# Kernel tuning notes

Hardware: AMD Instinct MI355X
Metric: run time of the kernel (lower is better)

The kernel has to match this reference:

```python
import jax, jax.numpy as jnp
import numpy as np

B, T, D, H = 16, 512, 512, 16
DH = D // H
P = 2 * T - 1  # relative position length


def _conv2d_same(x, w, b):
    # x: [B,C,H,W], w: [O,I,3,3]
    y = jax.lax.conv_general_dilated(x, w, (1, 1), 'SAME',
                                     dimension_numbers=('NCHW', 'OIHW', 'NCHW'))
    return y + b[None, :, None, None]


def _relative_shift(ps):
    # ps: [B,H,T,P] -> pad, reshape trick, keep first P//2+1 == T columns
    b, h, t, p = ps.shape
    ps = jnp.pad(ps, ((0, 0), (0, 0), (0, 0), (1, 0)))
    ps = ps.reshape(b, h, p + 1, t)[:, :, 1:].reshape(b, h, t, p)
    return ps[..., : p // 2 + 1]


def setup_inputs() -> dict:
    key = jax.random.key(0)
    ks = jax.random.split(key, 20)
    s = 0.02
    return {
        'query': jax.random.normal(ks[0], (B, T, D), jnp.float32),
        'key': jax.random.normal(ks[1], (B, T, D), jnp.float32),
        'value': jax.random.normal(ks[2], (B, T, D), jnp.float32),
        'pos_embedding': jax.random.normal(ks[3], (B, P, D), jnp.float32),
        'mask': jax.random.bernoulli(ks[4], 0.1, (B, 1, T)),
        'bpp': jax.random.uniform(ks[5], (B, T, T), jnp.float32),
        'Wq': jax.random.normal(ks[6], (D, D), jnp.float32) * s,
        'bq': jnp.zeros((D,), jnp.float32),
        'Wk': jax.random.normal(ks[7], (D, D), jnp.float32) * s,
        'bk': jnp.zeros((D,), jnp.float32),
        'Wv': jax.random.normal(ks[8], (D, D), jnp.float32) * s,
        'bv': jnp.zeros((D,), jnp.float32),
        'Wp': jax.random.normal(ks[9], (D, D), jnp.float32) * s,
        'Wo': jax.random.normal(ks[10], (D, D), jnp.float32) * s,
        'bo': jnp.zeros((D,), jnp.float32),
        'u_bias': jax.random.normal(ks[11], (H, DH), jnp.float32) * s,
        'v_bias': jax.random.normal(ks[12], (H, DH), jnp.float32) * s,
        'c1w': jax.random.normal(ks[13], (16, 1, 3, 3), jnp.float32) * s,
        'c1b': jnp.zeros((16,), jnp.float32),
        'c2w': jax.random.normal(ks[14], (1, 16, 3, 3), jnp.float32) * s,
        'c2b': jnp.zeros((1,), jnp.float32),
    }


def reference(query, key, value, pos_embedding, mask, bpp,
              Wq, bq, Wk, bk, Wv, bv, Wp, Wo, bo,
              u_bias, v_bias, c1w, c1b, c2w, c2b):
    b = value.shape[0]
    # bpp-derived bias: [B,1,T,T]
    h1 = jax.nn.relu(_conv2d_same(bpp[:, None], c1w, c1b))
    bpp_bias = _conv2d_same(h1, c2w, c2b)  # broadcasts over heads

    q = (query @ Wq.T + bq).reshape(b, -1, H, DH)          # [B,T,H,dh]
    k = (key @ Wk.T + bk).reshape(b, -1, H, DH)            # [B,T,H,dh]
    v = (value @ Wv.T + bv).reshape(b, -1, H, DH)          # [B,T,H,dh]
    p = (pos_embedding @ Wp) .reshape(b, -1, H, DH) if False else (pos_embedding @ Wp.T).reshape(b, -1, H, DH)  # [B,P,H,dh]

    content_score = jnp.einsum('bthd,bshd->bhts', q + u_bias, k)
    pos_score = jnp.einsum('bthd,bphd->bhtp', q + v_bias, p)
    pos_score = _relative_shift(pos_score)                 # [B,H,T,T]

    score = (content_score + pos_score) / jnp.sqrt(jnp.asarray(DH, score_dtype := content_score.dtype)) + bpp_bias
    score = jnp.where(mask[:, None], jnp.asarray(-10000.0, score.dtype), score)
    attn = jax.nn.softmax(score, axis=-1)                  # dropout_p=0 (eval)

    ctx = jnp.einsum('bhts,bshd->bthd', attn, v).reshape(b, -1, D)
    return ctx @ Wo.T + bo
```

## Files before the change

### kernel.cpp

```cpp
#include <hip/hip_runtime.h>

constexpr int Bn  = 16;
constexpr int Tn  = 512;
constexpr int Dn  = 512;
constexpr int Hn  = 16;
constexpr int DHn = 32;
constexpr int Pn  = 1023;
constexpr size_t wE = (size_t)Dn * Dn;

typedef __attribute__((ext_vector_type(8))) short s16x8;
typedef __attribute__((ext_vector_type(4))) float f32x4;

__device__ __forceinline__ unsigned short f2bf(float x) {
    unsigned u = __float_as_uint(x);
    unsigned r = u + 0x7fff + ((u >> 16) & 1);
    return (unsigned short)(r >> 16);
}
__device__ __forceinline__ float bf2f(unsigned short h) {
    return __uint_as_float(((unsigned)h) << 16);
}

__device__ __forceinline__ f32x4 mfma3(s16x8 ah, s16x8 al, s16x8 bh2, s16x8 bl, f32x4 c) {
    c = __builtin_amdgcn_mfma_f32_16x16x32_bf16(ah, bh2, c, 0, 0, 0);
    c = __builtin_amdgcn_mfma_f32_16x16x32_bf16(ah, bl,  c, 0, 0, 0);
    c = __builtin_amdgcn_mfma_f32_16x16x32_bf16(al, bh2, c, 0, 0, 0);
    return c;
}

__global__ __launch_bounds__(256) void split_weights_kernel(
    const float* __restrict__ w0, const float* __restrict__ w1,
    const float* __restrict__ w2, const float* __restrict__ w3,
    const float* __restrict__ w4,
    unsigned short* __restrict__ hi, unsigned short* __restrict__ lo) {
    const float* srcs[5] = {w0, w1, w2, w3, w4};
    const float* src = srcs[blockIdx.y];
    const size_t off = (size_t)blockIdx.y * wE;
    unsigned short* h = hi + off;
    unsigned short* l = lo + off;
    const int n4 = Dn * Dn / 4;
    for (int i = blockIdx.x * 256 + threadIdx.x; i < n4; i += 64 * 256) {
        float4 v = ((const float4*)src)[i];
        ushort4 hh, ll;
        hh.x = f2bf(v.x); ll.x = f2bf(v.x - bf2f(hh.x));
        hh.y = f2bf(v.y); ll.y = f2bf(v.y - bf2f(hh.y));
        hh.z = f2bf(v.z); ll.z = f2bf(v.z - bf2f(hh.z));
        hh.w = f2bf(v.w); ll.w = f2bf(v.w - bf2f(hh.w));
        ((ushort4*)h)[i] = hh;
        ((ushort4*)l)[i] = ll;
    }
}

__global__ void mask_decode_kernel(const unsigned char* __restrict__ mraw,
                                   float* __restrict__ mout) {
    __shared__ int s_nonmod4;
    __shared__ int s_big;
    if (threadIdx.x == 0) { s_nonmod4 = 0; s_big = 0; }
    __syncthreads();
    int f0 = 0, f1 = 0;
    for (int i = threadIdx.x; i < Bn * Tn; i += 256) {
        unsigned char v = mraw[i];
        if ((i & 3) != 0 && v != 0) f0 = 1;
        if (v > 1) f1 = 1;
    }
    if (f0) atomicOr(&s_nonmod4, 1);
    if (f1) atomicOr(&s_big, 1);
    __syncthreads();
    const int layout = s_big ? 2 : (s_nonmod4 ? 1 : 0);
    for (int i = threadIdx.x; i < Bn * Tn; i += 256) {
        bool m;
        if (layout == 2)      m = ((const float*)mraw)[i] != 0.0f;
        else if (layout == 1) m = mraw[i] != 0;
        else                  m = ((const int*)mraw)[i] != 0;
        mout[i] = m ? 1.0f : 0.0f;
    }
}

__global__ __launch_bounds__(256) void conv_bias_kernel(
    const float* __restrict__ bpp, const float* __restrict__ c1w,
    const float* __restrict__ c1b, const float* __restrict__ c2w,
    const float* __restrict__ c2b, unsigned short* __restrict__ biasout) {
    const int x0 = blockIdx.x * 64, y0 = blockIdx.y * 64, b = blockIdx.z;
    __shared__ __align__(16) float inb[68][72];
    __shared__ __align__(16) float h1[66][72];
    __shared__ float w1s[16][9], w2s[16][9], b1s[16];
    const int tid = threadIdx.x;
    const int tx = tid & 15, ty = tid >> 4;

    if (tid < 144) { w1s[tid / 9][tid % 9] = c1w[tid]; w2s[tid / 9][tid % 9] = c2w[tid]; }
    if (tid < 16) b1s[tid] = c1b[tid];
    const float* src = bpp + (size_t)b * Tn * Tn;
    for (int i = tid; i < 68 * 18; i += 256) {
        const int r = i / 18, cq = i % 18;
        const int gy = y0 - 2 + r, gx = x0 - 4 + cq * 4;
        float4 v = make_float4(0.f, 0.f, 0.f, 0.f);
        if (gy >= 0 && gy < Tn && gx >= 0 && gx < Tn)
            v = *(const float4*)(src + (size_t)gy * Tn + gx);
        *(float4*)&inb[r][cq * 4] = v;
    }
    __syncthreads();

    float acc[4][4] = {};
    for (int ch = 0; ch < 16; ++ch) {
        if (ch) __syncthreads();
        float w1r[9], w2r[9];
#pragma unroll
        for (int k = 0; k < 9; ++k) { w1r[k] = w1s[ch][k]; w2r[k] = w2s[ch][k]; }
        const float b1v = b1s[ch];
        for (int i = tid; i < 66 * 17; i += 256) {
            const int rr = i / 17, q = i % 17;
            float v[3][8];
#pragma unroll
            for (int dy = 0; dy < 3; ++dy) {
                float4 p0 = *(const float4*)&inb[rr + dy][q * 4];
                float4 p1 = *(const float4*)&inb[rr + dy][q * 4 + 4];
                v[dy][0] = p0.x; v[dy][1] = p0.y; v[dy][2] = p0.z; v[dy][3] = p0.w;
                v[dy][4] = p1.x; v[dy][5] = p1.y; v[dy][6] = p1.z; v[dy][7] = p1.w;
            }
            const int gy = y0 + rr - 1;
            const int gxb = x0 + q * 4 - 1;
            const bool rowok = (gy >= 0 && gy < Tn);
            float o4[4];
#pragma unroll
            for (int j = 0; j < 4; ++j) {
                float s = b1v;
#pragma unroll
                for (int dy = 0; dy < 3; ++dy)
#pragma unroll
                    for (int dx = 0; dx < 3; ++dx)
                        s += v[dy][2 + j + dx] * w1r[dy * 3 + dx];
                const int gx = gxb + j;
                o4[j] = (rowok && gx >= 0 && gx < Tn) ? fmaxf(s, 0.0f) : 0.0f;
            }
            *(float4*)&h1[rr][q * 4] = make_float4(o4[0], o4[1], o4[2], o4[3]);
        }
        __syncthreads();
        float h[6][6];
#pragma unroll
        for (int r6 = 0; r6 < 6; ++r6) {
            float4 a = *(const float4*)&h1[ty * 4 + r6][tx * 4];
            float2 b2 = *(const float2*)&h1[ty * 4 + r6][tx * 4 + 4];
            h[r6][0] = a.x; h[r6][1] = a.y; h[r6][2] = a.z; h[r6][3] = a.w;
            h[r6][4] = b2.x; h[r6][5] = b2.y;
        }
#pragma unroll
        for (int i2 = 0; i2 < 4; ++i2)
#pragma unroll
            for (int j = 0; j < 4; ++j) {
                float s = 0.0f;
#pragma unroll
                for (int dy = 0; dy < 3; ++dy)
#pragma unroll
                    for (int dx = 0; dx < 3; ++dx)
                        s += h[i2 + dy][j + dx] * w2r[dy * 3 + dx];
                acc[i2][j] += s;
            }
    }
    const float ob = c2b[0];
#pragma unroll
    for (int i2 = 0; i2 < 4; ++i2) {
        ushort4 o;
        o.x = f2bf(acc[i2][0] + ob); o.y = f2bf(acc[i2][1] + ob);
        o.z = f2bf(acc[i2][2] + ob); o.w = f2bf(acc[i2][3] + ob);
        *(ushort4*)(biasout + ((size_t)b * Tn + y0 + ty * 4 + i2) * Tn + x0 + tx * 4) = o;
    }
}

template<int NT>
__device__ __forceinline__ void gemm_body(
    const float* __restrict__ A,
    const unsigned short* __restrict__ Wh, const unsigned short* __restrict__ Wl,
    const float* __restrict__ bias, float* __restrict__ outf,
    unsigned short* __restrict__ out_hi, unsigned short* __restrict__ out_lo,
    int M, int L, int mode, int nbase, int mbase) {
    constexpr int K = 512, BK = 32, LDT = 40, NW = NT / 32;
    constexpr int WC = (NT * BK) / (256 * 8);
    __shared__ __align__(16) unsigned short AhT[128 * LDT];
    __shared__ __align__(16) unsigned short AlT[128 * LDT];
    __shared__ __align__(16) unsigned short WhT[NT * LDT];
    __shared__ __align__(16) unsigned short WlT[NT * LDT];
    const int tid = threadIdx.x;
    const int wave = tid >> 6, lane = tid & 63;
    const int wr = wave >> 1, wc = wave & 1;
    const int lg = lane >> 4, lr = lane & 15;
    f32x4 acc[4][NW] = {};

    float4 pa0[2], pa1[2];
    s16x8 pwh[WC], pwl[WC];
    auto issue_loads = [&](int k0) {
#pragma unroll
        for (int c = 0; c < 2; ++c) {
            const int cid = tid + 256 * c;
            const int row = cid >> 2, col8 = (cid & 3) * 8;
            int gm = mbase + row; if (gm >= M) gm = M - 1;
            const float* ap = A + (size_t)gm * K + k0 + col8;
            pa0[c] = *(const float4*)ap;
            pa1[c] = *(const float4*)(ap + 4);
        }
#pragma unroll
        for (int c = 0; c < WC; ++c) {
            const int cid = tid + 256 * c;
            const int row = cid >> 2, col8 = (cid & 3) * 8;
            const size_t gw = (size_t)(nbase + row) * K + k0 + col8;
            pwh[c] = *(const s16x8*)&Wh[gw];
            pwl[c] = *(const s16x8*)&Wl[gw];
        }
    };
    issue_loads(0);
    for (int ks = 0; ks < K / BK; ++ks) {
        const int k0 = ks * BK;
        __syncthreads();
#pragma unroll
        for (int c = 0; c < 2; ++c) {
            const int cid = tid + 256 * c;
            const int row = cid >> 2, col8 = (cid & 3) * 8;
            float av[8] = {pa0[c].x, pa0[c].y, pa0[c].z, pa0[c].w,
                           pa1[c].x, pa1[c].y, pa1[c].z, pa1[c].w};
            s16x8 hh, ll;
#pragma unroll
            for (int j = 0; j < 8; ++j) {
                unsigned short x = f2bf(av[j]);
                hh[j] = (short)x;
                ll[j] = (short)f2bf(av[j] - bf2f(x));
            }
            const int loff = row * LDT + col8;
            *(s16x8*)&AhT[loff] = hh;
            *(s16x8*)&AlT[loff] = ll;
        }
#pragma unroll
        for (int c = 0; c < WC; ++c) {
            const int cid = tid + 256 * c;
            const int loff = (cid >> 2) * LDT + (cid & 3) * 8;
            *(s16x8*)&WhT[loff] = pwh[c];
            *(s16x8*)&WlT[loff] = pwl[c];
        }
        if (ks < K / BK - 1) issue_loads(k0 + BK);
        __syncthreads();
        s16x8 wh[NW], wl[NW];
#pragma unroll
        for (int nj = 0; nj < NW; ++nj) {
            const int off = (wc * (NT / 2) + nj * 16 + lr) * LDT + lg * 8;
            wh[nj] = *(const s16x8*)&WhT[off];
            wl[nj] = *(const s16x8*)&WlT[off];
        }
#pragma unroll
        for (int mi = 0; mi < 4; ++mi) {
            const int off = (wr * 64 + mi * 16 + lr) * LDT + lg * 8;
            s16x8 ah = *(const s16x8*)&AhT[off];
            s16x8 al = *(const s16x8*)&AlT[off];
#pragma unroll
            for (int nj = 0; nj < NW; ++nj)
                acc[mi][nj] = __builtin_amdgcn_mfma_f32_16x16x32_bf16(ah, wh[nj], acc[mi][nj], 0, 0, 0);
#pragma unroll
            for (int nj = 0; nj < NW; ++nj)
                acc[mi][nj] = __builtin_amdgcn_mfma_f32_16x16x32_bf16(ah, wl[nj], acc[mi][nj], 0, 0, 0);
#pragma unroll
            for (int nj = 0; nj < NW; ++nj)
                acc[mi][nj] = __builtin_amdgcn_mfma_f32_16x16x32_bf16(al, wh[nj], acc[mi][nj], 0, 0, 0);
        }
    }
#pragma unroll
    for (int nj = 0; nj < NW; ++nj) {
        const int n = nbase + wc * (NT / 2) + nj * 16 + lr;
        const float bv = bias ? bias[n] : 0.0f;
#pragma unroll
        for (int mi = 0; mi < 4; ++mi) {
#pragma unroll
            for (int r2 = 0; r2 < 4; ++r2) {
                const int m = mbase + wr * 64 + mi * 16 + lg * 4 + r2;
                if (m < M) {
                    const float v = acc[mi][nj][r2] + bv;
                    if (mode == 0) {
                        outf[(size_t)m * 512 + n] = v;
                    } else if (mode == 1) {
                        int bb = m / L, t = m - bb * L;
                        int hh2 = n >> 5, d = n & 31;
                        outf[(((size_t)bb * Hn + hh2) * L + t) * DHn + d] = v;
                    } else {
                        int bb = m / L, t = m - bb * L;
                        int hh2 = n >> 5, d = n & 31;
                        size_t oidx = (mode == 2)
                            ? ((((size_t)bb * Hn + hh2) * L + t) * DHn + d)
                            : ((((size_t)bb * Hn + hh2) * DHn + d) * L + t);
                        unsigned short hi16 = f2bf(v);
                        out_hi[oidx] = hi16;
                        out_lo[oidx] = f2bf(v - bf2f(hi16));
                    }
                }
            }
        }
    }
}

__global__ __launch_bounds__(256, 3) void gemm_qkvp_kernel(
    const float* __restrict__ q, const float* __restrict__ k,
    const float* __restrict__ v, const float* __restrict__ p,
    const unsigned short* __restrict__ wall_hi, const unsigned short* __restrict__ wall_lo,
    const float* __restrict__ bq, const float* __restrict__ bk,
    const float* __restrict__ bv,
    float* __restrict__ q_ws,
    unsigned short* __restrict__ k_hi, unsigned short* __restrict__ k_lo,
    unsigned short* __restrict__ v_hi, unsigned short* __restrict__ v_lo,
    unsigned short* __restrict__ p_hi, unsigned short* __restrict__ p_lo) {
    const int bid = blockIdx.x;
    const int swz = (bid & 7) * 160 + (bid >> 3);
    int z, mblk, nblk;
    if (swz < 768) { z = swz >> 8; const int r = swz & 255; mblk = r >> 2; nblk = r & 3; }
    else           { z = 3; const int r = swz - 768;        mblk = r >> 2; nblk = r & 3; }
    const float* A; const float* bias = nullptr;
    float* outf = nullptr; unsigned short *ohi = nullptr, *olo = nullptr;
    int M, L, mode;
    if (z == 0)      { A = q; bias = bq; outf = q_ws; M = Bn * Tn; L = Tn; mode = 1; }
    else if (z == 1) { A = k; bias = bk; ohi = k_hi; olo = k_lo; M = Bn * Tn; L = Tn; mode = 2; }
    else if (z == 2) { A = v; bias = bv; ohi = v_hi; olo = v_lo; M = Bn * Tn; L = Tn; mode = 3; }
    else             { A = p; ohi = p_hi; olo = p_lo; M = Bn * Pn; L = Pn; mode = 2; }
    gemm_body<128>(A, wall_hi + (size_t)z * wE, wall_lo + (size_t)z * wE, bias,
                   outf, ohi, olo, M, L, mode, nblk * 128, mblk * 128);
}

__global__ __launch_bounds__(256, 3) void gemm_o_kernel(
    const float* __restrict__ A,
    const unsigned short* __restrict__ Wh, const unsigned short* __restrict__ Wl,
    const float* __restrict__ bias, float* __restrict__ out) {
    const int bid = blockIdx.x;
    const int swz = (bid & 7) * 64 + (bid >> 3);
    const int nbase = (swz & 7) * 64;
    const int mbase = (swz >> 3) * 128;
    gemm_body<64>(A, Wh, Wl, bias, out, nullptr, nullptr,
                  Bn * Tn, Tn, 0, nbase, mbase);
}

__global__ __launch_bounds__(256, 2) void attn_mfma_kernel(
    const float* __restrict__ q_ws,
    const unsigned short* __restrict__ k_hi, const unsigned short* __restrict__ k_lo,
    const unsigned short* __restrict__ vt_hi, const unsigned short* __restrict__ vt_lo,
    const unsigned short* __restrict__ p_hi, const unsigned short* __restrict__ p_lo,
    const unsigned short* __restrict__ biasw, const float* __restrict__ maskw,
    const float* __restrict__ ub, const float* __restrict__ vb,
    float* __restrict__ ctx) {
    const int bid = blockIdx.x;
    const int wg = ((bid & 7) << 9) | (bid >> 3);
    const int t0 = (wg & 15) * 32;
    const int h = (wg >> 4) & 15;
    const int b = wg >> 8;
    const int tid = threadIdx.x;
    const int w = tid >> 6, l = tid & 63;
    const int lr = l & 15, lg = l >> 4;
    const size_t bh = (size_t)b * Hn + h;
    const int pbase = 480 - t0;
    const float scale = 0.17677669529663687f;

    __shared__ __align__(16) char uni[4][8192];
    __shared__ float redbuf[2][32][4];
    char* ubase = uni[w];

    s16x8 quh[2], qul[2], qvh[2], qvl[2];
#pragma unroll
    for (int i = 0; i < 2; ++i) {
        const float* qrow = q_ws + (bh * Tn + t0 + 16 * i + lr) * DHn + lg * 8;
        float4 qa = *(const float4*)qrow;
        float4 qb = *(const float4*)(qrow + 4);
        float qv8[8] = {qa.x, qa.y, qa.z, qa.w, qb.x, qb.y, qb.z, qb.w};
#pragma unroll
        for (int j = 0; j < 8; ++j) {
            const float uj = ub[h * DHn + lg * 8 + j];
            const float vj = vb[h * DHn + lg * 8 + j];
            float xu = qv8[j] + uj;
            unsigned short hu = f2bf(xu);
            quh[i][j] = (short)hu; qul[i][j] = (short)f2bf(xu - bf2f(hu));
            float xv = qv8[j] + vj;
            unsigned short hv = f2bf(xv);
            qvh[i][j] = (short)hv; qvl[i][j] = (short)f2bf(xv - bf2f(hv));
        }
    }
    float mv[8];
#pragma unroll
    for (int m = 0; m < 8; ++m)
        mv[m] = maskw[b * Tn + w * 128 + m * 16 + lr];

    auto posTile = [&](int i, int jt) -> f32x4 {
        int pidx = pbase + w * 128 + jt * 16 + lr;
        if (pidx > Pn - 1) pidx = Pn - 1;
        const size_t po = (bh * Pn + pidx) * DHn + lg * 8;
        s16x8 ph = *(const s16x8*)(p_hi + po);
        s16x8 pl = *(const s16x8*)(p_lo + po);
        f32x4 t = {0.f, 0.f, 0.f, 0.f};
        return mfma3(qvh[i], qvl[i], ph, pl, t);
    };

    f32x4 sc[2][8];
    f32x4 p0a = posTile(0, 1);
    f32x4 p1a = posTile(1, 0);
    const int ubb = lr - 4 * lg + 31;

#pragma unroll
    for (int m = 0; m < 8; ++m) {
        f32x4 p0b = posTile(0, m + 2);
        f32x4 p1b = posTile(1, m + 1);
        float bvls[2][4];
#pragma unroll
        for (int i2 = 0; i2 < 2; ++i2)
#pragma unroll
            for (int r2 = 0; r2 < 4; ++r2)
                bvls[i2][r2] = bf2f(biasw[((size_t)b * Tn + t0 + 16 * i2 + 4 * lg + r2) * Tn
                                          + w * 128 + m * 16 + lr]);
        const size_t ko = (bh * Tn + w * 128 + m * 16 + lr) * DHn + lg * 8;
        s16x8 kh = *(const s16x8*)(k_hi + ko);
        s16x8 kl = *(const s16x8*)(k_lo + ko);
#pragma unroll
        for (int i = 0; i < 2; ++i) {
            f32x4 c = {0.f, 0.f, 0.f, 0.f};
            c = mfma3(quh[i], qul[i], kh, kl, c);
            f32x4 Pa = (i == 0) ? p0a : p1a;
            f32x4 Pb = (i == 0) ? p0b : p1b;
            f32x4 out;
#pragma unroll
            for (int r2 = 0; r2 < 4; ++r2) {
                const int u = ubb - r2;
                const int src = (l & 48) | (u & 15);
                float pa = __shfl(Pa[r2], src, 64);
                float pb = __shfl(Pb[r2], src, 64);
                float pv = (u < 32) ? pa : pb;
                float v = (c[r2] + pv) * scale + bvls[i][r2];
                if (mv[m] != 0.0f) v = -10000.0f;
                out[r2] = v;
            }
            sc[i][m] = out;
        }
        p0a = p0b; p1a = p1b;
    }

    float rowm[2][4], inv[2][4];
#pragma unroll
    for (int i = 0; i < 2; ++i)
#pragma unroll
        for (int r2 = 0; r2 < 4; ++r2) {
            float mx = -1e30f;
#pragma unroll
            for (int m = 0; m < 8; ++m) mx = fmaxf(mx, sc[i][m][r2]);
#pragma unroll
            for (int off = 1; off < 16; off <<= 1) mx = fmaxf(mx, __shfl_xor(mx, off, 64));
            if (lr == 0) redbuf[0][16 * i + 4 * lg + r2][w] = mx;
        }
    __syncthreads();
#pragma unroll
    for (int i = 0; i < 2; ++i)
#pragma unroll
        for (int r2 = 0; r2 < 4; ++r2) {
            float4 mm = *(const float4*)redbuf[0][16 * i + 4 * lg + r2];
            rowm[i][r2] = fmaxf(fmaxf(mm.x, mm.y), fmaxf(mm.z, mm.w));
        }
    float psum[2][4] = {};
#pragma unroll
    for (int i = 0; i < 2; ++i)
#pragma unroll
        for (int m = 0; m < 8; ++m)
#pragma unroll
            for (int r2 = 0; r2 < 4; ++r2) {
                float e = __expf(sc[i][m][r2] - rowm[i][r2]);
                sc[i][m][r2] = e;
                psum[i][r2] += e;
            }
#pragma unroll
    for (int i = 0; i < 2; ++i)
#pragma unroll
        for (int r2 = 0; r2 < 4; ++r2) {
            float s = psum[i][r2];
#pragma unroll
            for (int off = 1; off < 16; off <<= 1) s += __shfl_xor(s, off, 64);
            if (lr == 0) redbuf[1][16 * i + 4 * lg + r2][w] = s;
        }
    __syncthreads();
#pragma unroll
    for (int i = 0; i < 2; ++i)
#pragma unroll
        for (int r2 = 0; r2 < 4; ++r2) {
            float4 ss = *(const float4*)redbuf[1][16 * i + 4 * lg + r2];
            inv[i][r2] = 1.0f / (ss.x + ss.y + ss.z + ss.w);
        }

    f32x4 cacc[2][2] = {};
#pragma unroll
    for (int sh = 0; sh < 2; ++sh) {
#pragma unroll
        for (int mm2 = 0; mm2 < 4; ++mm2) {
            const int m = sh * 4 + mm2;
#pragma unroll
            for (int i = 0; i < 2; ++i)
#pragma unroll
                for (int r2 = 0; r2 < 4; ++r2) {
                    const int trow = 16 * i + 4 * lg + r2;
                    float a = sc[i][m][r2] * inv[i][r2];
                    unsigned short ah16 = f2bf(a);
                    unsigned short al16 = f2bf(a - bf2f(ah16));
                    const int cbyte = (mm2 * 16 + lr) * 2;
                    const int off = trow * 128 + (cbyte ^ ((trow & 7) << 4));
                    *(unsigned short*)(ubase + off) = ah16;
                    *(unsigned short*)(ubase + 4096 + off) = al16;
                }
        }
#pragma unroll
        for (int ks = 0; ks < 2; ++ks) {
            s16x8 pah[2], pal[2];
#pragma unroll
            for (int i = 0; i < 2; ++i) {
                const int trow = 16 * i + lr;
                const int cbyte = ks * 64 + lg * 16;
                const int off = trow * 128 + (cbyte ^ ((trow & 7) << 4));
                pah[i] = *(const s16x8*)(ubase + off);
                pal[i] = *(const s16x8*)(ubase + 4096 + off);
            }
#pragma unroll
            for (int n = 0; n < 2; ++n) {
                const int sg = w * 128 + sh * 64 + ks * 32 + lg * 8;
                const size_t vo = (bh * DHn + n * 16 + lr) * Tn + sg;
                s16x8 vh = *(const s16x8*)(vt_hi + vo);
                s16x8 vl = *(const s16x8*)(vt_lo + vo);
#pragma unroll
                for (int i = 0; i < 2; ++i)
                    cacc[i][n] = mfma3(pah[i], pal[i], vh, vl, cacc[i][n]);
            }
        }
    }

    {
        float* cr = (float*)ubase;
#pragma unroll
        for (int i = 0; i < 2; ++i)
#pragma unroll
            for (int n = 0; n < 2; ++n)
#pragma unroll
                for (int r2 = 0; r2 < 4; ++r2)
                    cr[(16 * i + 4 * lg + r2) * 36 + n * 16 + lr] = cacc[i][n][r2];
    }
    __syncthreads();
    {
        const int trow = tid >> 3, d0 = (tid & 7) * 4;
        float4 s0 = *(const float4*)((float*)uni[0] + trow * 36 + d0);
        float4 s1 = *(const float4*)((float*)uni[1] + trow * 36 + d0);
        float4 s2 = *(const float4*)((float*)uni[2] + trow * 36 + d0);
        float4 s3 = *(const float4*)((float*)uni[3] + trow * 36 + d0);
        float4 o = make_float4(s0.x + s1.x + s2.x + s3.x, s0.y + s1.y + s2.y + s3.y,
                               s0.z + s1.z + s2.z + s3.z, s0.w + s1.w + s2.w + s3.w);
        *(float4*)(ctx + ((size_t)b * Tn + t0 + trow) * Dn + h * DHn + d0) = o;
    }
}

extern "C" void kernel_launch(void* const* d_in, const int* in_sizes, int n_in,
                              void* d_out, int out_size, void* d_ws, size_t ws_size,
                              hipStream_t stream) {
    const float* query = (const float*)d_in[0];
    const float* key   = (const float*)d_in[1];
    const float* value = (const float*)d_in[2];
    const float* pos   = (const float*)d_in[3];
    const unsigned char* mask = (const unsigned char*)d_in[4];
    const float* bpp = (const float*)d_in[5];
    const float* Wq = (const float*)d_in[6];
    const float* bq = (const float*)d_in[7];
    const float* Wk = (const float*)d_in[8];
    const float* bk = (const float*)d_in[9];
    const float* Wv = (const float*)d_in[10];
    const float* bv = (const float*)d_in[11];
    const float* Wp = (const float*)d_in[12];
    const float* Wo = (const float*)d_in[13];
    const float* bo = (const float*)d_in[14];
    const float* ub = (const float*)d_in[15];
    const float* vbias = (const float*)d_in[16];
    const float* c1w = (const float*)d_in[17];
    const float* c1b = (const float*)d_in[18];
    const float* c2w = (const float*)d_in[19];
    const float* c2b = (const float*)d_in[20];

    const size_t qkvE = (size_t)Bn * Hn * Tn * DHn;
    const size_t posE = (size_t)Bn * Hn * Pn * DHn;

    char* wsb = (char*)d_ws;
    unsigned short* bias_ws = (unsigned short*)wsb;
    float* mask_ws = (float*)(wsb + sizeof(unsigned short) * (size_t)Bn * Tn * Tn);
    float* q_ws    = mask_ws + Bn * Tn;
    float* ctx_ws  = q_ws + qkvE;
    unsigned short* k_hi = (unsigned short*)(ctx_ws + (size_t)Bn * Tn * Dn);
    unsigned short* k_lo = k_hi + qkvE;
    unsigned short* v_hi = k_lo + qkvE;
    unsigned short* v_lo = v_hi + qkvE;
    unsigned short* p_hi = v_lo + qkvE;
    unsigned short* p_lo = p_hi + posE;
    unsigned short* wall_hi = p_lo + posE;
    unsigned short* wall_lo = wall_hi + 5 * wE;

    split_weights_kernel<<<dim3(64, 5), dim3(256), 0, stream>>>(
        Wq, Wk, Wv, Wp, Wo, wall_hi, wall_lo);
    mask_decode_kernel<<<dim3(1), dim3(256), 0, stream>>>(mask, mask_ws);
    conv_bias_kernel<<<dim3(8, 8, Bn), dim3(256), 0, stream>>>(
        bpp, c1w, c1b, c2w, c2b, bias_ws);

    gemm_qkvp_kernel<<<dim3(1280), dim3(256), 0, stream>>>(
        query, key, value, pos, wall_hi, wall_lo, bq, bk, bv,
        q_ws, k_hi, k_lo, v_hi, v_lo, p_hi, p_lo);

    attn_mfma_kernel<<<dim3(4096), dim3(256), 0, stream>>>(
        q_ws, k_hi, k_lo, v_hi, v_lo, p_hi, p_lo, bias_ws, mask_ws, ub, vbias, ctx_ws);

    gemm_o_kernel<<<dim3(512), dim3(256), 0, stream>>>(
        ctx_ws, wall_hi + 4 * wE, wall_lo + 4 * wE, bo, (float*)d_out);
}
```

Measured before the change: 416.3 us.

## Merge conv bias, mask decode and QKVP GEMM into one launch

Folds the bpp convolution kernel and the mask decode kernel into the QKVP projection kernel as extra blocks, using a shared-memory arena overlaid between the GEMM and conv layouts. This removes two launches and lets the conv work fill idle CUs during the GEMM tail. In exchange, the conv blocks now run under the GEMM's launch bounds and shared memory size, which may change their occupancy and register allocation. The single mask block can also land at the end of the grid.

```diff
diff --git a/kernel.cpp b/kernel.cpp
--- a/kernel.cpp
+++ b/kernel.cpp
@@ -50,123 +50,23 @@
     }
 }
 
-__global__ void mask_decode_kernel(const unsigned char* __restrict__ mraw,
-                                   float* __restrict__ mout) {
-    __shared__ int s_nonmod4;
-    __shared__ int s_big;
-    if (threadIdx.x == 0) { s_nonmod4 = 0; s_big = 0; }
-    __syncthreads();
-    int f0 = 0, f1 = 0;
-    for (int i = threadIdx.x; i < Bn * Tn; i += 256) {
-        unsigned char v = mraw[i];
-        if ((i & 3) != 0 && v != 0) f0 = 1;
-        if (v > 1) f1 = 1;
-    }
-    if (f0) atomicOr(&s_nonmod4, 1);
-    if (f1) atomicOr(&s_big, 1);
-    __syncthreads();
-    const int layout = s_big ? 2 : (s_nonmod4 ? 1 : 0);
-    for (int i = threadIdx.x; i < Bn * Tn; i += 256) {
-        bool m;
-        if (layout == 2)      m = ((const float*)mraw)[i] != 0.0f;
-        else if (layout == 1) m = mraw[i] != 0;
-        else                  m = ((const int*)mraw)[i] != 0;
-        mout[i] = m ? 1.0f : 0.0f;
-    }
-}
-
-__global__ __launch_bounds__(256) void conv_bias_kernel(
-    const float* __restrict__ bpp, const float* __restrict__ c1w,
-    const float* __restrict__ c1b, const float* __restrict__ c2w,
-    const float* __restrict__ c2b, unsigned short* __restrict__ biasout) {
-    const int x0 = blockIdx.x * 64, y0 = blockIdx.y * 64, b = blockIdx.z;
-    __shared__ __align__(16) float inb[68][72];
-    __shared__ __align__(16) float h1[66][72];
-    __shared__ float w1s[16][9], w2s[16][9], b1s[16];
-    const int tid = threadIdx.x;
-    const int tx = tid & 15, ty = tid >> 4;
-
-    if (tid < 144) { w1s[tid / 9][tid % 9] = c1w[tid]; w2s[tid / 9][tid % 9] = c2w[tid]; }
-    if (tid < 16) b1s[tid] = c1b[tid];
-    const float* src = bpp + (size_t)b * Tn * Tn;
-    for (int i = tid; i < 68 * 18; i += 256) {
-        const int r = i / 18, cq = i % 18;
-        const int gy = y0 - 2 + r, gx = x0 - 4 + cq * 4;
-        float4 v = make_float4(0.f, 0.f, 0.f, 0.f);
-        if (gy >= 0 && gy < Tn && gx >= 0 && gx < Tn)
-            v = *(const float4*)(src + (size_t)gy * Tn + gx);
-        *(float4*)&inb[r][cq * 4] = v;
-    }
-    __syncthreads();
-
-    float acc[4][4] = {};
-    for (int ch = 0; ch < 16; ++ch) {
-        if (ch) __syncthreads();
-        float w1r[9], w2r[9];
-#pragma unroll
-        for (int k = 0; k < 9; ++k) { w1r[k] = w1s[ch][k]; w2r[k] = w2s[ch][k]; }
-        const float b1v = b1s[ch];
-        for (int i = tid; i < 66 * 17; i += 256) {
-            const int rr = i / 17, q = i % 17;
-            float v[3][8];
-#pragma unroll
-            for (int dy = 0; dy < 3; ++dy) {
-                float4 p0 = *(const float4*)&inb[rr + dy][q * 4];
-                float4 p1 = *(const float4*)&inb[rr + dy][q * 4 + 4];
-                v[dy][0] = p0.x; v[dy][1] = p0.y; v[dy][2] = p0.z; v[dy][3] = p0.w;
-                v[dy][4] = p1.x; v[dy][5] = p1.y; v[dy][6] = p1.z; v[dy][7] = p1.w;
-            }
-            const int gy = y0 + rr - 1;
-            const int gxb = x0 + q * 4 - 1;
-            const bool rowok = (gy >= 0 && gy < Tn);
-            float o4[4];
-#pragma unroll
-            for (int j = 0; j < 4; ++j) {
-                float s = b1v;
-#pragma unroll
-                for (int dy = 0; dy < 3; ++dy)
-#pragma unroll
-                    for (int dx = 0; dx < 3; ++dx)
-                        s += v[dy][2 + j + dx] * w1r[dy * 3 + dx];
-                const int gx = gxb + j;
-                o4[j] = (rowok && gx >= 0 && gx < Tn) ? fmaxf(s, 0.0f) : 0.0f;
-            }
-            *(float4*)&h1[rr][q * 4] = make_float4(o4[0], o4[1], o4[2], o4[3]);
-        }
-        __syncthreads();
-        float h[6][6];
-#pragma unroll
-        for (int r6 = 0; r6 < 6; ++r6) {
-            float4 a = *(const float4*)&h1[ty * 4 + r6][tx * 4];
-            float2 b2 = *(const float2*)&h1[ty * 4 + r6][tx * 4 + 4];
-            h[r6][0] = a.x; h[r6][1] = a.y; h[r6][2] = a.z; h[r6][3] = a.w;
-            h[r6][4] = b2.x; h[r6][5] = b2.y;
-        }
-#pragma unroll
-        for (int i2 = 0; i2 < 4; ++i2)
-#pragma unroll
-            for (int j = 0; j < 4; ++j) {
-                float s = 0.0f;
-#pragma unroll
-                for (int dy = 0; dy < 3; ++dy)
-#pragma unroll
-                    for (int dx = 0; dx < 3; ++dx)
-                        s += h[i2 + dy][j + dx] * w2r[dy * 3 + dx];
-                acc[i2][j] += s;
-            }
-    }
-    const float ob = c2b[0];
-#pragma unroll
-    for (int i2 = 0; i2 < 4; ++i2) {
-        ushort4 o;
-        o.x = f2bf(acc[i2][0] + ob); o.y = f2bf(acc[i2][1] + ob);
-        o.z = f2bf(acc[i2][2] + ob); o.w = f2bf(acc[i2][3] + ob);
-        *(ushort4*)(biasout + ((size_t)b * Tn + y0 + ty * 4 + i2) * Tn + x0 + tx * 4) = o;
-    }
-}
+struct GemmSmem {
+    unsigned short AhT[128 * 40];
+    unsigned short AlT[128 * 40];
+    unsigned short WhT[128 * 40];
+    unsigned short WlT[128 * 40];
+};
+struct ConvSmem {
+    float inb[68][72];
+    float h1[66][72];
+    float w1s[16][9], w2s[16][9], b1s[16];
+};
+static_assert(sizeof(ConvSmem) <= sizeof(GemmSmem), "arena too small");
 
 template<int NT>
 __device__ __forceinline__ void gemm_body(
+    unsigned short* __restrict__ AhT, unsigned short* __restrict__ AlT,
+    unsigned short* __restrict__ WhT, unsigned short* __restrict__ WlT,
     const float* __restrict__ A,
     const unsigned short* __restrict__ Wh, const unsigned short* __restrict__ Wl,
     const float* __restrict__ bias, float* __restrict__ outf,
@@ -174,10 +74,6 @@
     int M, int L, int mode, int nbase, int mbase) {
     constexpr int K = 512, BK = 32, LDT = 40, NW = NT / 32;
     constexpr int WC = (NT * BK) / (256 * 8);
-    __shared__ __align__(16) unsigned short AhT[128 * LDT];
-    __shared__ __align__(16) unsigned short AlT[128 * LDT];
-    __shared__ __align__(16) unsigned short WhT[NT * LDT];
-    __shared__ __align__(16) unsigned short WlT[NT * LDT];
     const int tid = threadIdx.x;
     const int wave = tid >> 6, lane = tid & 63;
     const int wr = wave >> 1, wc = wave & 1;
@@ -291,7 +187,7 @@
     }
 }
 
-__global__ __launch_bounds__(256, 3) void gemm_qkvp_kernel(
+__global__ __launch_bounds__(256, 3) void phase1_kernel(
     const float* __restrict__ q, const float* __restrict__ k,
     const float* __restrict__ v, const float* __restrict__ p,
     const unsigned short* __restrict__ wall_hi, const unsigned short* __restrict__ wall_lo,
@@ -300,32 +196,157 @@
     float* __restrict__ q_ws,
     unsigned short* __restrict__ k_hi, unsigned short* __restrict__ k_lo,
     unsigned short* __restrict__ v_hi, unsigned short* __restrict__ v_lo,
-    unsigned short* __restrict__ p_hi, unsigned short* __restrict__ p_lo) {
+    unsigned short* __restrict__ p_hi, unsigned short* __restrict__ p_lo,
+    const float* __restrict__ bpp, const float* __restrict__ c1w,
+    const float* __restrict__ c1b, const float* __restrict__ c2w,
+    const float* __restrict__ c2b, unsigned short* __restrict__ biasout,
+    const unsigned char* __restrict__ mraw, float* __restrict__ mout) {
+    __shared__ __align__(16) char arena[sizeof(GemmSmem)];
     const int bid = blockIdx.x;
-    const int swz = (bid & 7) * 160 + (bid >> 3);
-    int z, mblk, nblk;
-    if (swz < 768) { z = swz >> 8; const int r = swz & 255; mblk = r >> 2; nblk = r & 3; }
-    else           { z = 3; const int r = swz - 768;        mblk = r >> 2; nblk = r & 3; }
-    const float* A; const float* bias = nullptr;
-    float* outf = nullptr; unsigned short *ohi = nullptr, *olo = nullptr;
-    int M, L, mode;
-    if (z == 0)      { A = q; bias = bq; outf = q_ws; M = Bn * Tn; L = Tn; mode = 1; }
-    else if (z == 1) { A = k; bias = bk; ohi = k_hi; olo = k_lo; M = Bn * Tn; L = Tn; mode = 2; }
-    else if (z == 2) { A = v; bias = bv; ohi = v_hi; olo = v_lo; M = Bn * Tn; L = Tn; mode = 3; }
-    else             { A = p; ohi = p_hi; olo = p_lo; M = Bn * Pn; L = Pn; mode = 2; }
-    gemm_body<128>(A, wall_hi + (size_t)z * wE, wall_lo + (size_t)z * wE, bias,
-                   outf, ohi, olo, M, L, mode, nblk * 128, mblk * 128);
+    const int tid = threadIdx.x;
+
+    if (bid < 1280) {
+        GemmSmem* gs = (GemmSmem*)arena;
+        const int swz = (bid & 7) * 160 + (bid >> 3);
+        int z, mblk, nblk;
+        if (swz < 768) { z = swz >> 8; const int r = swz & 255; mblk = r >> 2; nblk = r & 3; }
+        else           { z = 3; const int r = swz - 768;        mblk = r >> 2; nblk = r & 3; }
+        const float* A; const float* bias = nullptr;
+        float* outf = nullptr; unsigned short *ohi = nullptr, *olo = nullptr;
+        int M, L, mode;
+        if (z == 0)      { A = q; bias = bq; outf = q_ws; M = Bn * Tn; L = Tn; mode = 1; }
+        else if (z == 1) { A = k; bias = bk; ohi = k_hi; olo = k_lo; M = Bn * Tn; L = Tn; mode = 2; }
+        else if (z == 2) { A = v; bias = bv; ohi = v_hi; olo = v_lo; M = Bn * Tn; L = Tn; mode = 3; }
+        else             { A = p; ohi = p_hi; olo = p_lo; M = Bn * Pn; L = Pn; mode = 2; }
+        gemm_body<128>(gs->AhT, gs->AlT, gs->WhT, gs->WlT,
+                       A, wall_hi + (size_t)z * wE, wall_lo + (size_t)z * wE, bias,
+                       outf, ohi, olo, M, L, mode, nblk * 128, mblk * 128);
+        return;
+    }
+    if (bid < 1280 + 1024) {
+        ConvSmem* cs = (ConvSmem*)arena;
+        const int cid = bid - 1280;
+        const int b = cid >> 6, rem = cid & 63;
+        const int x0 = (rem & 7) * 64, y0 = (rem >> 3) * 64;
+        const int tx = tid & 15, ty = tid >> 4;
+
+        if (tid < 144) { cs->w1s[tid / 9][tid % 9] = c1w[tid]; cs->w2s[tid / 9][tid % 9] = c2w[tid]; }
+        if (tid < 16) cs->b1s[tid] = c1b[tid];
+        const float* src = bpp + (size_t)b * Tn * Tn;
+        for (int i = tid; i < 68 * 18; i += 256) {
+            const int r = i / 18, cq = i % 18;
+            const int gy = y0 - 2 + r, gx = x0 - 4 + cq * 4;
+            float4 vv = make_float4(0.f, 0.f, 0.f, 0.f);
+            if (gy >= 0 && gy < Tn && gx >= 0 && gx < Tn)
+                vv = *(const float4*)(src + (size_t)gy * Tn + gx);
+            *(float4*)&cs->inb[r][cq * 4] = vv;
+        }
+        __syncthreads();
+
+        float acc[4][4] = {};
+        for (int ch = 0; ch < 16; ++ch) {
+            if (ch) __syncthreads();
+            float w1r[9], w2r[9];
+#pragma unroll
+            for (int kk = 0; kk < 9; ++kk) { w1r[kk] = cs->w1s[ch][kk]; w2r[kk] = cs->w2s[ch][kk]; }
+            const float b1v = cs->b1s[ch];
+            for (int i = tid; i < 66 * 17; i += 256) {
+                const int rr = i / 17, qq = i % 17;
+                float vv[3][8];
+#pragma unroll
+                for (int dy = 0; dy < 3; ++dy) {
+                    float4 p0 = *(const float4*)&cs->inb[rr + dy][qq * 4];
+                    float4 p1 = *(const float4*)&cs->inb[rr + dy][qq * 4 + 4];
+                    vv[dy][0] = p0.x; vv[dy][1] = p0.y; vv[dy][2] = p0.z; vv[dy][3] = p0.w;
+                    vv[dy][4] = p1.x; vv[dy][5] = p1.y; vv[dy][6] = p1.z; vv[dy][7] = p1.w;
+                }
+                const int gy = y0 + rr - 1;
+                const int gxb = x0 + qq * 4 - 1;
+                const bool rowok = (gy >= 0 && gy < Tn);
+                float o4[4];
+#pragma unroll
+                for (int j = 0; j < 4; ++j) {
+                    float s = b1v;
+#pragma unroll
+                    for (int dy = 0; dy < 3; ++dy)
+#pragma unroll
+                        for (int dx = 0; dx < 3; ++dx)
+                            s += vv[dy][2 + j + dx] * w1r[dy * 3 + dx];
+                    const int gx = gxb + j;
+                    o4[j] = (rowok && gx >= 0 && gx < Tn) ? fmaxf(s, 0.0f) : 0.0f;
+                }
+                *(float4*)&cs->h1[rr][qq * 4] = make_float4(o4[0], o4[1], o4[2], o4[3]);
+            }
+            __syncthreads();
+            float hh[6][6];
+#pragma unroll
+            for (int r6 = 0; r6 < 6; ++r6) {
+                float4 a = *(const float4*)&cs->h1[ty * 4 + r6][tx * 4];
+                float2 b2 = *(const float2*)&cs->h1[ty * 4 + r6][tx * 4 + 4];
+                hh[r6][0] = a.x; hh[r6][1] = a.y; hh[r6][2] = a.z; hh[r6][3] = a.w;
+                hh[r6][4] = b2.x; hh[r6][5] = b2.y;
+            }
+#pragma unroll
+            for (int i2 = 0; i2 < 4; ++i2)
+#pragma unroll
+                for (int j = 0; j < 4; ++j) {
+                    float s = 0.0f;
+#pragma unroll
+                    for (int dy = 0; dy < 3; ++dy)
+#pragma unroll
+                        for (int dx = 0; dx < 3; ++dx)
+                            s += hh[i2 + dy][j + dx] * w2r[dy * 3 + dx];
+                    acc[i2][j] += s;
+                }
+        }
+        const float ob = c2b[0];
+#pragma unroll
+        for (int i2 = 0; i2 < 4; ++i2) {
+            ushort4 o;
+            o.x = f2bf(acc[i2][0] + ob); o.y = f2bf(acc[i2][1] + ob);
+            o.z = f2bf(acc[i2][2] + ob); o.w = f2bf(acc[i2][3] + ob);
+            *(ushort4*)(biasout + ((size_t)b * Tn + y0 + ty * 4 + i2) * Tn + x0 + tx * 4) = o;
+        }
+        return;
+    }
+    {
+        int* flags = (int*)arena;
+        if (tid == 0) { flags[0] = 0; flags[1] = 0; }
+        __syncthreads();
+        int f0 = 0, f1 = 0;
+        for (int i = tid; i < Bn * Tn; i += 256) {
+            unsigned char vv = mraw[i];
+            if ((i & 3) != 0 && vv != 0) f0 = 1;
+            if (vv > 1) f1 = 1;
+        }
+        if (f0) atomicOr(&flags[0], 1);
+        if (f1) atomicOr(&flags[1], 1);
+        __syncthreads();
+        const int layout = flags[1] ? 2 : (flags[0] ? 1 : 0);
+        for (int i = tid; i < Bn * Tn; i += 256) {
+            bool m;
+            if (layout == 2)      m = ((const float*)mraw)[i] != 0.0f;
+            else if (layout == 1) m = mraw[i] != 0;
+            else                  m = ((const int*)mraw)[i] != 0;
+            mout[i] = m ? 1.0f : 0.0f;
+        }
+    }
 }
 
 __global__ __launch_bounds__(256, 3) void gemm_o_kernel(
     const float* __restrict__ A,
     const unsigned short* __restrict__ Wh, const unsigned short* __restrict__ Wl,
     const float* __restrict__ bias, float* __restrict__ out) {
+    constexpr int LDT = 40;
+    __shared__ __align__(16) unsigned short AhT[128 * LDT];
+    __shared__ __align__(16) unsigned short AlT[128 * LDT];
+    __shared__ __align__(16) unsigned short WhT[64 * LDT];
+    __shared__ __align__(16) unsigned short WlT[64 * LDT];
     const int bid = blockIdx.x;
     const int swz = (bid & 7) * 64 + (bid >> 3);
     const int nbase = (swz & 7) * 64;
     const int mbase = (swz >> 3) * 128;
-    gemm_body<64>(A, Wh, Wl, bias, out, nullptr, nullptr,
+    gemm_body<64>(AhT, AlT, WhT, WlT, A, Wh, Wl, bias, out, nullptr, nullptr,
                   Bn * Tn, Tn, 0, nbase, mbase);
 }
 
@@ -589,13 +610,11 @@
 
     split_weights_kernel<<<dim3(64, 5), dim3(256), 0, stream>>>(
         Wq, Wk, Wv, Wp, Wo, wall_hi, wall_lo);
-    mask_decode_kernel<<<dim3(1), dim3(256), 0, stream>>>(mask, mask_ws);
-    conv_bias_kernel<<<dim3(8, 8, Bn), dim3(256), 0, stream>>>(
-        bpp, c1w, c1b, c2w, c2b, bias_ws);
-
-    gemm_qkvp_kernel<<<dim3(1280), dim3(256), 0, stream>>>(
+
+    phase1_kernel<<<dim3(1280 + 1024 + 1), dim3(256), 0, stream>>>(
         query, key, value, pos, wall_hi, wall_lo, bq, bk, bv,
-        q_ws, k_hi, k_lo, v_hi, v_lo, p_hi, p_lo);
+        q_ws, k_hi, k_lo, v_hi, v_lo, p_hi, p_lo,
+        bpp, c1w, c1b, c2w, c2b, bias_ws, mask, mask_ws);
 
     attn_mfma_kernel<<<dim3(4096), dim3(256), 0, stream>>>(
         q_ws, k_hi, k_lo, v_hi, v_lo, p_hi, p_lo, bias_ws, mask_ws, ub, vbias, ctx_ws);
```

Result: faster. 369.5 us (-11.2%).
